# Kernel tuning notes

Hardware: AMD Instinct MI355X
Metric: run time of the kernel (lower is better)

## Reference

```python
import jax, jax.numpy as jnp
import numpy as np

N_NODES = 100000
N_EDGES = 1600000
INPUT_DIM, HIDDEN_DIM, OUTPUT_DIM = 128, 256, 2
BN_EPS = 1e-5


def setup_inputs() -> dict:
    key = jax.random.key(0)
    ks = jax.random.split(key, 8)
    x = jax.random.normal(ks[0], (N_NODES, INPUT_DIM), jnp.float32)
    edge_index = jax.random.randint(ks[1], (2, N_EDGES), 0, N_NODES, dtype=jnp.int32).astype(jnp.int64)
    # Glorot-ish init for GCNConv weights; PyG GCNConv has bias by default.
    def glorot(k, fan_in, fan_out):
        s = jnp.sqrt(6.0 / (fan_in + fan_out))
        return jax.random.uniform(k, (fan_in, fan_out), jnp.float32, -s, s)
    return {
        "x": x,
        "edge_index": edge_index,
        "W0": glorot(ks[2], INPUT_DIM, HIDDEN_DIM),
        "b0": jnp.zeros((HIDDEN_DIM,), jnp.float32),
        "W1": glorot(ks[3], HIDDEN_DIM, HIDDEN_DIM),
        "b1": jnp.zeros((HIDDEN_DIM,), jnp.float32),
        "W2": glorot(ks[4], HIDDEN_DIM, OUTPUT_DIM),
        "b2": jnp.zeros((OUTPUT_DIM,), jnp.float32),
        "gamma0": jnp.ones((HIDDEN_DIM,), jnp.float32),
        "beta0": jnp.zeros((HIDDEN_DIM,), jnp.float32),
        "gamma1": jnp.ones((HIDDEN_DIM,), jnp.float32),
        "beta1": jnp.zeros((HIDDEN_DIM,), jnp.float32),
    }


def _gcn_norm(edge_index, num_nodes):
    # PyG gcn_norm: add self-loops, deg over destination, D^-1/2 A_hat D^-1/2
    loop = jnp.arange(num_nodes, dtype=edge_index.dtype)
    src = jnp.concatenate([edge_index[0], loop])
    dst = jnp.concatenate([edge_index[1], loop])
    deg = jax.ops.segment_sum(jnp.ones_like(dst, jnp.float32), dst, num_segments=num_nodes)
    dinv = jax.lax.rsqrt(jnp.maximum(deg, 1.0))  # deg >= 1 due to self-loops
    norm = dinv[src] * dinv[dst]  # [E + N]
    return src, dst, norm


def _gcn_conv(x, W, b, src, dst, norm, num_nodes):
    h = x @ W                          # [N, out] dense GEMM first (PyG order)
    msg = h[src] * norm[:, None]       # gather + edge scale
    out = jax.ops.segment_sum(msg, dst, num_segments=num_nodes)  # scatter-add
    return out + b


def _batchnorm(x, gamma, beta):
    # training-mode BatchNorm1d over nodes (biased variance, as torch uses for normalization)
    mean = jnp.mean(x, axis=0)
    var = jnp.mean(jnp.square(x - mean), axis=0)
    return (x - mean) * jax.lax.rsqrt(var + BN_EPS) * gamma + beta


def reference(x, edge_index, W0, b0, W1, b1, W2, b2, gamma0, beta0, gamma1, beta1):
    n = x.shape[0]
    src, dst, norm = _gcn_norm(edge_index, n)
    h = _gcn_conv(x, W0, b0, src, dst, norm, n)
    h = jax.nn.relu(_batchnorm(h, gamma0, beta0))  # dropout is identity (eval / deterministic)
    h = _gcn_conv(h, W1, b1, src, dst, norm, n)
    h = jax.nn.relu(_batchnorm(h, gamma1, beta1))
    out = _gcn_conv(h, W2, b2, src, dst, norm, n)
    return out
```

## Files before the change

### kernel.cpp

```cpp
#include <hip/hip_runtime.h>
#include <hip/hip_fp16.h>


#define BN_EPS 1e-5f

union HF4 { float4 f; __half2 h[4]; };

typedef __attribute__((ext_vector_type(8))) _Float16 f16x8;
typedef __attribute__((ext_vector_type(4))) float f32x4;

__global__ void detect_i64(const unsigned int* __restrict__ w, int* flag) {
  __shared__ unsigned int red[256];
  unsigned int v = 0;
  int t = threadIdx.x;
  for (int i = t; i < 1024; i += 256) v |= w[2 * i + 1];
  red[t] = v;
  __syncthreads();
  for (int s = 128; s > 0; s >>= 1) {
    if (t < s) red[t] |= red[t + s];
    __syncthreads();
  }
  if (t == 0) *flag = (red[0] == 0u) ? 1 : 0;
}

__global__ void convert_deg(const unsigned int* __restrict__ w, const int* __restrict__ flag,
                            int* __restrict__ srcI, int* __restrict__ dstI,
                            int* __restrict__ deg, int E) {
  int i = blockIdx.x * blockDim.x + threadIdx.x;
  if (i >= E) return;
  int f = *flag;
  int s = (int)(f ? w[2 * (size_t)i] : w[i]);
  int d = (int)(f ? w[2 * ((size_t)E + i)] : w[(size_t)E + i]);
  srcI[i] = s;
  dstI[i] = d;
  atomicAdd(&deg[d], 1);
}

__global__ void make_dinv(const int* __restrict__ deg, float* __restrict__ dinv, int N) {
  int i = blockIdx.x * blockDim.x + threadIdx.x;
  if (i < N) dinv[i] = rsqrtf((float)deg[i] + 1.0f);
}

__global__ void scan_partial(const int* __restrict__ deg, int* __restrict__ blksum, int N) {
  __shared__ int s[256];
  int b = blockIdx.x, t = threadIdx.x;
  int base = b * 1024 + t * 4;
  int v = 0;
#pragma unroll
  for (int k = 0; k < 4; ++k) {
    int i = base + k;
    if (i < N) v += deg[i];
  }
  s[t] = v;
  __syncthreads();
  for (int st = 128; st > 0; st >>= 1) {
    if (t < st) s[t] += s[t + st];
    __syncthreads();
  }
  if (t == 0) blksum[b] = s[0];
}

__global__ void scan_blk(int* __restrict__ blksum, int B) {
  __shared__ int s[256];
  int t = threadIdx.x;
  int v = (t < B) ? blksum[t] : 0;
  s[t] = v;
  __syncthreads();
  for (int off = 1; off < 256; off <<= 1) {
    int u = (t >= off) ? s[t - off] : 0;
    __syncthreads();
    s[t] += u;
    __syncthreads();
  }
  if (t < B) blksum[t] = s[t] - v;
}

__global__ void scan_final(const int* __restrict__ deg, const int* __restrict__ blkoff,
                           int* __restrict__ rowptr, int N, int E) {
  __shared__ int s[256];
  int b = blockIdx.x, t = threadIdx.x;
  int base = b * 1024 + t * 4;
  int v[4];
  int sum = 0;
#pragma unroll
  for (int k = 0; k < 4; ++k) {
    int i = base + k;
    v[k] = (i < N) ? deg[i] : 0;
    sum += v[k];
  }
  s[t] = sum;
  __syncthreads();
  for (int off = 1; off < 256; off <<= 1) {
    int u = (t >= off) ? s[t - off] : 0;
    __syncthreads();
    s[t] += u;
    __syncthreads();
  }
  int ex = s[t] - sum + blkoff[b];
#pragma unroll
  for (int k = 0; k < 4; ++k) {
    int i = base + k;
    if (i < N) {
      rowptr[i] = ex;
      ex += v[k];
    }
  }
  if (b == 0 && t == 0) rowptr[N] = E;
}

__global__ void csr_scatter(const int* __restrict__ src, const int* __restrict__ dst,
                            const float* __restrict__ dinv, const int* __restrict__ rowptr,
                            int* __restrict__ fill, int* __restrict__ col,
                            float* __restrict__ wgt, int E) {
  int e = blockIdx.x * blockDim.x + threadIdx.x;
  if (e >= E) return;
  int s = src[e], d = dst[e];
  int pos = atomicAdd(&fill[d], 1);
  int slot = rowptr[d] + pos;
  col[slot] = s;
  wgt[slot] = dinv[s] * dinv[d];
}

__global__ void f32_to_f16(const float4* __restrict__ in, float4* __restrict__ outh, long n8) {
  long t = (long)blockIdx.x * blockDim.x + threadIdx.x;
  if (t >= n8) return;
  float4 a = in[2 * t], b = in[2 * t + 1];
  HF4 o;
  o.h[0] = __floats2half2_rn(a.x, a.y);
  o.h[1] = __floats2half2_rn(a.z, a.w);
  o.h[2] = __floats2half2_rn(b.x, b.y);
  o.h[3] = __floats2half2_rn(b.z, b.w);
  outh[t] = o.f;
}

__global__ void pack_w(const float* __restrict__ W, _Float16* __restrict__ Wp, int K, int NC) {
  int idx = blockIdx.x * blockDim.x + threadIdx.x;
  if (idx >= K * NC) return;
  int k = idx / NC, n = idx - k * NC;
  int kb = k >> 5, kk = k & 31, seg = kk >> 3, j = kk & 7;
  Wp[(((kb * 4 + seg) * NC) + n) * 8 + j] = (_Float16)W[idx];
}

template <int LPN>
__global__ void agg_gather_h(const float4* __restrict__ inh, float4* __restrict__ outh,
                             const int* __restrict__ rowptr, const int* __restrict__ col,
                             const float* __restrict__ wgt, const float* __restrict__ dinv,
                             int N) {
  long g = (long)blockIdx.x * blockDim.x + threadIdx.x;
  int n = (int)(g / LPN);
  int lane = (int)(g & (LPN - 1));
  if (n >= N) return;
  float ws = dinv[n];
  ws *= ws;
  float acc[8];
  {
    HF4 u;
    u.f = inh[(long)n * LPN + lane];
#pragma unroll
    for (int i = 0; i < 4; ++i) {
      float2 f = __half22float2(u.h[i]);
      acc[2 * i] = ws * f.x;
      acc[2 * i + 1] = ws * f.y;
    }
  }
  int beg = rowptr[n], end = rowptr[n + 1];
  int j = beg;
  for (; j + 3 < end; j += 4) {
    int s0 = col[j], s1 = col[j + 1], s2 = col[j + 2], s3 = col[j + 3];
    float w0 = wgt[j], w1 = wgt[j + 1], w2 = wgt[j + 2], w3 = wgt[j + 3];
    HF4 a, b, c, d;
    a.f = inh[(long)s0 * LPN + lane];
    b.f = inh[(long)s1 * LPN + lane];
    c.f = inh[(long)s2 * LPN + lane];
    d.f = inh[(long)s3 * LPN + lane];
#pragma unroll
    for (int i = 0; i < 4; ++i) {
      float2 fa = __half22float2(a.h[i]);
      float2 fb = __half22float2(b.h[i]);
      float2 fc = __half22float2(c.h[i]);
      float2 fd = __half22float2(d.h[i]);
      acc[2 * i] += w0 * fa.x + w1 * fb.x + w2 * fc.x + w3 * fd.x;
      acc[2 * i + 1] += w0 * fa.y + w1 * fb.y + w2 * fc.y + w3 * fd.y;
    }
  }
  for (; j < end; ++j) {
    int s0 = col[j];
    float w0 = wgt[j];
    HF4 a;
    a.f = inh[(long)s0 * LPN + lane];
#pragma unroll
    for (int i = 0; i < 4; ++i) {
      float2 fa = __half22float2(a.h[i]);
      acc[2 * i] += w0 * fa.x;
      acc[2 * i + 1] += w0 * fa.y;
    }
  }
  HF4 o;
  o.h[0] = __floats2half2_rn(acc[0], acc[1]);
  o.h[1] = __floats2half2_rn(acc[2], acc[3]);
  o.h[2] = __floats2half2_rn(acc[4], acc[5]);
  o.h[3] = __floats2half2_rn(acc[6], acc[7]);
  outh[(long)n * LPN + lane] = o.f;
}

template <int K, int NC>
__global__ __launch_bounds__(256) void gemm_mfma(const _Float16* __restrict__ A,
                                                 const float4* __restrict__ Wpack,
                                                 _Float16* __restrict__ H,
                                                 float* __restrict__ gsum,
                                                 float* __restrict__ gsq, int M) {
  __shared__ float red0[NC];
  __shared__ float red1[NC];
  int tid = threadIdx.x;
  if (tid < NC) {
    red0[tid] = 0.f;
    red1[tid] = 0.f;
  }
  __syncthreads();
  int wave = tid >> 6;
  int lane = tid & 63;
  int row0 = (blockIdx.x * 4 + wave) * 32;
  bool active = row0 < M;
  int arow0 = active ? row0 : 0;
  int r = lane & 15;
  int seg = lane >> 4;
  f32x4 acc0[NC / 16], acc1[NC / 16];
#pragma unroll
  for (int t = 0; t < NC / 16; ++t) {
    acc0[t] = (f32x4){0.f, 0.f, 0.f, 0.f};
    acc1[t] = (f32x4){0.f, 0.f, 0.f, 0.f};
  }
  const _Float16* arowA = A + (long)(arow0 + r) * K;
  const _Float16* arowB = A + (long)(arow0 + 16 + r) * K;
#pragma unroll
  for (int k0 = 0; k0 < K; k0 += 32) {
    f16x8 af0 = *(const f16x8*)(arowA + k0 + seg * 8);
    f16x8 af1 = *(const f16x8*)(arowB + k0 + seg * 8);
    const float4* wp = Wpack + ((k0 >> 5) * 4 + seg) * NC;
#pragma unroll
    for (int t = 0; t < NC / 16; ++t) {
      f16x8 bf = *(const f16x8*)(wp + t * 16 + r);
      acc0[t] = __builtin_amdgcn_mfma_f32_16x16x32_f16(af0, bf, acc0[t], 0, 0, 0);
      acc1[t] = __builtin_amdgcn_mfma_f32_16x16x32_f16(af1, bf, acc1[t], 0, 0, 0);
    }
  }
#pragma unroll
  for (int t = 0; t < NC / 16; ++t) {
    int c = t * 16 + r;
    float s = 0.f, q = 0.f;
#pragma unroll
    for (int qq = 0; qq < 4; ++qq) {
      float v0 = acc0[t][qq], v1 = acc1[t][qq];
      s += v0 + v1;
      q += v0 * v0 + v1 * v1;
    }
    s += __shfl_xor(s, 16, 64);
    s += __shfl_xor(s, 32, 64);
    q += __shfl_xor(q, 16, 64);
    q += __shfl_xor(q, 32, 64);
    if (active) {
      if (seg == 0) {
        atomicAdd(&red0[c], s);
        atomicAdd(&red1[c], q);
      }
#pragma unroll
      for (int qq = 0; qq < 4; ++qq) {
        H[(long)(row0 + seg * 4 + qq) * NC + c] = (_Float16)acc0[t][qq];
        H[(long)(row0 + 16 + seg * 4 + qq) * NC + c] = (_Float16)acc1[t][qq];
      }
    }
  }
  __syncthreads();
  if (tid < NC) {
    atomicAdd(&gsum[tid], red0[tid]);
    atomicAdd(&gsq[tid], red1[tid]);
  }
}

__global__ void bn_finalize(const float* __restrict__ gsum, const float* __restrict__ gsq,
                            const float* __restrict__ gamma, const float* __restrict__ beta,
                            float* __restrict__ scale, float* __restrict__ shift, float invN) {
  int c = threadIdx.x;
  float mean = gsum[c] * invN;
  float var = fmaxf(gsq[c] * invN - mean * mean, 0.f);
  float sc = rsqrtf(var + BN_EPS) * gamma[c];
  scale[c] = sc;
  shift[c] = beta[c] - mean * sc;
}

__global__ void bn_apply_h(const float4* __restrict__ h_in, float4* __restrict__ h_out,
                           const float4* __restrict__ scale4, const float4* __restrict__ shift4,
                           long total8) {
  long t = (long)blockIdx.x * blockDim.x + threadIdx.x;
  if (t >= total8) return;
  HF4 u;
  u.f = h_in[t];
  int c8 = (int)(t & 31);
  float4 sc0 = scale4[2 * c8], sh0 = shift4[2 * c8];
  float4 sc1 = scale4[2 * c8 + 1], sh1 = shift4[2 * c8 + 1];
  float2 f0 = __half22float2(u.h[0]);
  float2 f1 = __half22float2(u.h[1]);
  float2 f2 = __half22float2(u.h[2]);
  float2 f3 = __half22float2(u.h[3]);
  HF4 o;
  o.h[0] = __floats2half2_rn(fmaxf(f0.x * sc0.x + sh0.x, 0.f), fmaxf(f0.y * sc0.y + sh0.y, 0.f));
  o.h[1] = __floats2half2_rn(fmaxf(f1.x * sc0.z + sh0.z, 0.f), fmaxf(f1.y * sc0.w + sh0.w, 0.f));
  o.h[2] = __floats2half2_rn(fmaxf(f2.x * sc1.x + sh1.x, 0.f), fmaxf(f2.y * sc1.y + sh1.y, 0.f));
  o.h[3] = __floats2half2_rn(fmaxf(f3.x * sc1.z + sh1.z, 0.f), fmaxf(f3.y * sc1.w + sh1.w, 0.f));
  h_out[t] = o.f;
}

__global__ void bn_apply_proj(const float4* __restrict__ h_in, const float* __restrict__ scale,
                              const float* __restrict__ shift, const float* __restrict__ W2,
                              float* __restrict__ P, int N) {
  int tid = threadIdx.x;
  int row = blockIdx.x * 8 + (tid >> 5);
  int lr = tid & 31;
  if (row >= N) return;
  HF4 u;
  u.f = h_in[(long)row * 32 + lr];
  int c0 = lr * 8;
  float s0 = 0.f, s1 = 0.f;
#pragma unroll
  for (int i = 0; i < 4; ++i) {
    float2 f = __half22float2(u.h[i]);
    int ca = c0 + 2 * i, cb = c0 + 2 * i + 1;
    float va = fmaxf(f.x * scale[ca] + shift[ca], 0.f);
    float vb = fmaxf(f.y * scale[cb] + shift[cb], 0.f);
    s0 += va * W2[2 * ca] + vb * W2[2 * cb];
    s1 += va * W2[2 * ca + 1] + vb * W2[2 * cb + 1];
  }
#pragma unroll
  for (int off = 16; off > 0; off >>= 1) {
    s0 += __shfl_down(s0, off, 32);
    s1 += __shfl_down(s1, off, 32);
  }
  if (lr == 0) {
    P[2 * row] = s0;
    P[2 * row + 1] = s1;
  }
}

__global__ void final_gather(const float* __restrict__ P, float* __restrict__ out,
                             const int* __restrict__ rowptr, const int* __restrict__ col,
                             const float* __restrict__ wgt, const float* __restrict__ dinv,
                             const float* __restrict__ b2, int N) {
  int n = blockIdx.x * blockDim.x + threadIdx.x;
  if (n >= N) return;
  float w = dinv[n] * dinv[n];
  float a0 = w * P[2 * n + 0];
  float a1 = w * P[2 * n + 1];
  int end = rowptr[n + 1];
  for (int j = rowptr[n]; j < end; ++j) {
    int s = col[j];
    float ww = wgt[j];
    a0 += ww * P[2 * s + 0];
    a1 += ww * P[2 * s + 1];
  }
  out[2 * n + 0] = a0 + b2[0];
  out[2 * n + 1] = a1 + b2[1];
}

extern "C" void kernel_launch(void* const* d_in, const int* in_sizes, int n_in,
                              void* d_out, int out_size, void* d_ws, size_t ws_size,
                              hipStream_t stream) {
  const float* x = (const float*)d_in[0];
  const void* eidx = d_in[1];
  const float* W0 = (const float*)d_in[2];
  const float* W1 = (const float*)d_in[4];
  const float* W2 = (const float*)d_in[6];
  const float* b2 = (const float*)d_in[7];
  const float* gamma0 = (const float*)d_in[8];
  const float* beta0 = (const float*)d_in[9];
  const float* gamma1 = (const float*)d_in[10];
  const float* beta1 = (const float*)d_in[11];

  const int N = in_sizes[0] / 128;
  const int E = in_sizes[1] / 2;
  float* out = (float*)d_out;

  char* base = (char*)d_ws;
  size_t off = 0;
  auto alloc = [&](size_t bytes) {
    size_t o = off;
    off = (off + bytes + 255) & ~(size_t)255;
    return o;
  };
  const size_t o_col = alloc((size_t)E * 4);
  const size_t o_wgt = alloc((size_t)E * 4);
  const size_t o_rowptr = alloc((size_t)(N + 1) * 4);
  const size_t o_deg = alloc((size_t)N * 4);
  const size_t o_fill = alloc((size_t)N * 4);
  const size_t o_dinv = alloc((size_t)N * 4);
  const size_t o_blk = alloc(1024 * 4);
  const size_t o_flag = alloc(256);
  const size_t o_stats = alloc(4096);
  const size_t o_P = alloc((size_t)N * 2 * 4);
  const size_t o_W0p = alloc(128 * 256 * 2);
  const size_t o_W1p = alloc(256 * 256 * 2);
  const size_t o_H1 = alloc((size_t)N * 256 * 2);
  const size_t o_H2 = alloc((size_t)N * 256 * 2);

  int* col = (int*)(base + o_col);
  float* wgt = (float*)(base + o_wgt);
  int* rowptr = (int*)(base + o_rowptr);
  int* deg = (int*)(base + o_deg);
  int* fill = (int*)(base + o_fill);
  float* dinv = (float*)(base + o_dinv);
  int* blk = (int*)(base + o_blk);
  int* flag = (int*)(base + o_flag);
  float* gsum = (float*)(base + o_stats);
  float* gsq = gsum + 256;
  float* scale = gsum + 512;
  float* shift = gsum + 768;
  float* P = (float*)(base + o_P);
  _Float16* W0p = (_Float16*)(base + o_W0p);
  _Float16* W1p = (_Float16*)(base + o_W1p);
  float4* H1 = (float4*)(base + o_H1);
  float4* H2 = (float4*)(base + o_H2);
  int* idx32 = (int*)(base + o_H2);
  int* srcI = idx32;
  int* dstI = idx32 + E;

  auto cdiv = [](long a, long b) { return (int)((a + b - 1) / b); };
  const float invN = 1.0f / (float)N;
  const int B1 = cdiv(N, 1024);

  hipLaunchKernelGGL(detect_i64, dim3(1), dim3(256), 0, stream, (const unsigned int*)eidx, flag);
  hipMemsetAsync(deg, 0, (size_t)N * 4, stream);
  hipMemsetAsync(fill, 0, (size_t)N * 4, stream);
  hipLaunchKernelGGL(convert_deg, dim3(cdiv(E, 256)), dim3(256), 0, stream,
                     (const unsigned int*)eidx, flag, srcI, dstI, deg, E);

  hipLaunchKernelGGL(make_dinv, dim3(cdiv(N, 256)), dim3(256), 0, stream, deg, dinv, N);
  hipLaunchKernelGGL(scan_partial, dim3(B1), dim3(256), 0, stream, deg, blk, N);
  hipLaunchKernelGGL(scan_blk, dim3(1), dim3(256), 0, stream, blk, B1);
  hipLaunchKernelGGL(scan_final, dim3(B1), dim3(256), 0, stream, deg, blk, rowptr, N, E);
  hipLaunchKernelGGL(csr_scatter, dim3(cdiv(E, 256)), dim3(256), 0, stream, srcI, dstI, dinv,
                     rowptr, fill, col, wgt, E);
  hipLaunchKernelGGL(pack_w, dim3(cdiv(128 * 256, 256)), dim3(256), 0, stream, W0, W0p, 128, 256);
  hipLaunchKernelGGL(pack_w, dim3(cdiv(256 * 256, 256)), dim3(256), 0, stream, W1, W1p, 256, 256);
  hipLaunchKernelGGL(f32_to_f16, dim3(cdiv((long)N * 16, 256)), dim3(256), 0, stream,
                     (const float4*)x, H1, (long)N * 16);

  hipLaunchKernelGGL((agg_gather_h<16>), dim3(cdiv((long)N * 16, 256)), dim3(256), 0, stream,
                     H1, H2, rowptr, col, wgt, dinv, N);
  hipMemsetAsync(gsum, 0, 2048, stream);
  hipLaunchKernelGGL((gemm_mfma<128, 256>), dim3(cdiv(N, 128)), dim3(256), 0, stream,
                     (const _Float16*)H2, (const float4*)W0p, (_Float16*)H1, gsum, gsq, N);

  hipLaunchKernelGGL(bn_finalize, dim3(1), dim3(256), 0, stream, gsum, gsq, gamma0, beta0, scale,
                     shift, invN);
  hipLaunchKernelGGL(bn_apply_h, dim3(cdiv((long)N * 32, 256)), dim3(256), 0, stream,
                     (const float4*)H1, H2, (const float4*)scale, (const float4*)shift,
                     (long)N * 32);

  hipLaunchKernelGGL((agg_gather_h<32>), dim3(cdiv((long)N * 32, 256)), dim3(256), 0, stream,
                     H2, H1, rowptr, col, wgt, dinv, N);
  hipMemsetAsync(gsum, 0, 2048, stream);
  hipLaunchKernelGGL((gemm_mfma<256, 256>), dim3(cdiv(N, 128)), dim3(256), 0, stream,
                     (const _Float16*)H1, (const float4*)W1p, (_Float16*)H2, gsum, gsq, N);

  hipLaunchKernelGGL(bn_finalize, dim3(1), dim3(256), 0, stream, gsum, gsq, gamma1, beta1, scale,
                     shift, invN);
  hipLaunchKernelGGL(bn_apply_proj, dim3(cdiv(N, 8)), dim3(256), 0, stream, (const float4*)H2,
                     scale, shift, W2, P, N);

  hipLaunchKernelGGL(final_gather, dim3(cdiv(N, 256)), dim3(256), 0, stream, P, out, rowptr, col,
                     wgt, dinv, b2, N);
}
```

Baseline: 597.5 us.

## Fuse BN-apply into gather, split BN stats from GEMM, drop index conversion

Several changes land together. The int32 src/dst conversion pass is removed, so the degree count and CSR scatter read the raw edge index directly. The BN statistics reduction moves out of the MFMA GEMM epilogue into a separate bn_stats kernel. The GEMM operands are swapped so each lane writes four contiguous fp16 values instead of scalar strided stores. The layer-0 BN+ReLU apply is folded into the second aggregation's loads, removing a full read/write pass of the hidden activations. The cost is one extra read of the GEMM output for stats, and the BN transform is now recomputed once per edge gather instead of once per node.

After: 664.0 us. 1.11x slower.

```diff
diff --git a/kernel.cpp b/kernel.cpp
--- a/kernel.cpp
+++ b/kernel.cpp
@@ -5,6 +5,7 @@
 #define BN_EPS 1e-5f
 
 union HF4 { float4 f; __half2 h[4]; };
+union HF2 { float2 f; __half2 h[2]; };
 
 typedef __attribute__((ext_vector_type(8))) _Float16 f16x8;
 typedef __attribute__((ext_vector_type(4))) float f32x4;
@@ -23,21 +24,19 @@
   if (t == 0) *flag = (red[0] == 0u) ? 1 : 0;
 }
 
-__global__ void convert_deg(const unsigned int* __restrict__ w, const int* __restrict__ flag,
-                            int* __restrict__ srcI, int* __restrict__ dstI,
-                            int* __restrict__ deg, int E) {
+__global__ void deg_count(const unsigned int* __restrict__ w, const int* __restrict__ flag,
+                          int* __restrict__ deg, int E) {
   int i = blockIdx.x * blockDim.x + threadIdx.x;
   if (i >= E) return;
   int f = *flag;
-  int s = (int)(f ? w[2 * (size_t)i] : w[i]);
   int d = (int)(f ? w[2 * ((size_t)E + i)] : w[(size_t)E + i]);
-  srcI[i] = s;
-  dstI[i] = d;
   atomicAdd(&deg[d], 1);
 }
 
-__global__ void make_dinv(const int* __restrict__ deg, float* __restrict__ dinv, int N) {
+__global__ void make_dinv(const int* __restrict__ deg, float* __restrict__ dinv,
+                          float* __restrict__ stats, int N) {
   int i = blockIdx.x * blockDim.x + threadIdx.x;
+  if (i < 512) stats[i] = 0.f;
   if (i < N) dinv[i] = rsqrtf((float)deg[i] + 1.0f);
 }
 
@@ -108,13 +107,15 @@
   if (b == 0 && t == 0) rowptr[N] = E;
 }
 
-__global__ void csr_scatter(const int* __restrict__ src, const int* __restrict__ dst,
+__global__ void csr_scatter(const unsigned int* __restrict__ w, const int* __restrict__ flag,
                             const float* __restrict__ dinv, const int* __restrict__ rowptr,
                             int* __restrict__ fill, int* __restrict__ col,
                             float* __restrict__ wgt, int E) {
   int e = blockIdx.x * blockDim.x + threadIdx.x;
   if (e >= E) return;
-  int s = src[e], d = dst[e];
+  int f = *flag;
+  int s = (int)(f ? w[2 * (size_t)e] : w[e]);
+  int d = (int)(f ? w[2 * ((size_t)E + e)] : w[(size_t)E + e]);
   int pos = atomicAdd(&fill[d], 1);
   int slot = rowptr[d] + pos;
   col[slot] = s;
@@ -141,27 +142,46 @@
   Wp[(((kb * 4 + seg) * NC) + n) * 8 + j] = (_Float16)W[idx];
 }
 
-template <int LPN>
+template <int LPN, bool BN>
 __global__ void agg_gather_h(const float4* __restrict__ inh, float4* __restrict__ outh,
                              const int* __restrict__ rowptr, const int* __restrict__ col,
                              const float* __restrict__ wgt, const float* __restrict__ dinv,
+                             const float* __restrict__ scale, const float* __restrict__ shift,
                              int N) {
   long g = (long)blockIdx.x * blockDim.x + threadIdx.x;
   int n = (int)(g / LPN);
   int lane = (int)(g & (LPN - 1));
   if (n >= N) return;
+  float sc[8], sh[8];
+  if (BN) {
+    int c0 = lane * 8;
+#pragma unroll
+    for (int i = 0; i < 8; ++i) {
+      sc[i] = scale[c0 + i];
+      sh[i] = shift[c0 + i];
+    }
+  }
+  auto xf = [&](const HF4& u, float* o) {
+#pragma unroll
+    for (int i = 0; i < 4; ++i) {
+      float2 f = __half22float2(u.h[i]);
+      o[2 * i] = f.x;
+      o[2 * i + 1] = f.y;
+    }
+    if (BN) {
+#pragma unroll
+      for (int i = 0; i < 8; ++i) o[i] = fmaxf(o[i] * sc[i] + sh[i], 0.f);
+    }
+  };
   float ws = dinv[n];
   ws *= ws;
-  float acc[8];
+  float acc[8], v[8];
   {
     HF4 u;
     u.f = inh[(long)n * LPN + lane];
-#pragma unroll
-    for (int i = 0; i < 4; ++i) {
-      float2 f = __half22float2(u.h[i]);
-      acc[2 * i] = ws * f.x;
-      acc[2 * i + 1] = ws * f.y;
-    }
+    xf(u, v);
+#pragma unroll
+    for (int i = 0; i < 8; ++i) acc[i] = ws * v[i];
   }
   int beg = rowptr[n], end = rowptr[n + 1];
   int j = beg;
@@ -173,27 +193,21 @@
     b.f = inh[(long)s1 * LPN + lane];
     c.f = inh[(long)s2 * LPN + lane];
     d.f = inh[(long)s3 * LPN + lane];
-#pragma unroll
-    for (int i = 0; i < 4; ++i) {
-      float2 fa = __half22float2(a.h[i]);
-      float2 fb = __half22float2(b.h[i]);
-      float2 fc = __half22float2(c.h[i]);
-      float2 fd = __half22float2(d.h[i]);
-      acc[2 * i] += w0 * fa.x + w1 * fb.x + w2 * fc.x + w3 * fd.x;
-      acc[2 * i + 1] += w0 * fa.y + w1 * fb.y + w2 * fc.y + w3 * fd.y;
-    }
+    float va[8], vb[8], vc[8], vd[8];
+    xf(a, va); xf(b, vb); xf(c, vc); xf(d, vd);
+#pragma unroll
+    for (int i = 0; i < 8; ++i)
+      acc[i] += w0 * va[i] + w1 * vb[i] + w2 * vc[i] + w3 * vd[i];
   }
   for (; j < end; ++j) {
     int s0 = col[j];
     float w0 = wgt[j];
     HF4 a;
     a.f = inh[(long)s0 * LPN + lane];
-#pragma unroll
-    for (int i = 0; i < 4; ++i) {
-      float2 fa = __half22float2(a.h[i]);
-      acc[2 * i] += w0 * fa.x;
-      acc[2 * i + 1] += w0 * fa.y;
-    }
+    float va[8];
+    xf(a, va);
+#pragma unroll
+    for (int i = 0; i < 8; ++i) acc[i] += w0 * va[i];
   }
   HF4 o;
   o.h[0] = __floats2half2_rn(acc[0], acc[1]);
@@ -206,22 +220,12 @@
 template <int K, int NC>
 __global__ __launch_bounds__(256) void gemm_mfma(const _Float16* __restrict__ A,
                                                  const float4* __restrict__ Wpack,
-                                                 _Float16* __restrict__ H,
-                                                 float* __restrict__ gsum,
-                                                 float* __restrict__ gsq, int M) {
-  __shared__ float red0[NC];
-  __shared__ float red1[NC];
+                                                 _Float16* __restrict__ H, int M) {
   int tid = threadIdx.x;
-  if (tid < NC) {
-    red0[tid] = 0.f;
-    red1[tid] = 0.f;
-  }
-  __syncthreads();
   int wave = tid >> 6;
   int lane = tid & 63;
   int row0 = (blockIdx.x * 4 + wave) * 32;
-  bool active = row0 < M;
-  int arow0 = active ? row0 : 0;
+  if (row0 >= M) return;
   int r = lane & 15;
   int seg = lane >> 4;
   f32x4 acc0[NC / 16], acc1[NC / 16];
@@ -230,54 +234,66 @@
     acc0[t] = (f32x4){0.f, 0.f, 0.f, 0.f};
     acc1[t] = (f32x4){0.f, 0.f, 0.f, 0.f};
   }
-  const _Float16* arowA = A + (long)(arow0 + r) * K;
-  const _Float16* arowB = A + (long)(arow0 + 16 + r) * K;
+  int ra = min(row0 + r, M - 1);
+  int rb = min(row0 + 16 + r, M - 1);
+  const _Float16* arowA = A + (long)ra * K;
+  const _Float16* arowB = A + (long)rb * K;
 #pragma unroll
   for (int k0 = 0; k0 < K; k0 += 32) {
-    f16x8 af0 = *(const f16x8*)(arowA + k0 + seg * 8);
-    f16x8 af1 = *(const f16x8*)(arowB + k0 + seg * 8);
+    f16x8 hf0 = *(const f16x8*)(arowA + k0 + seg * 8);
+    f16x8 hf1 = *(const f16x8*)(arowB + k0 + seg * 8);
     const float4* wp = Wpack + ((k0 >> 5) * 4 + seg) * NC;
 #pragma unroll
     for (int t = 0; t < NC / 16; ++t) {
-      f16x8 bf = *(const f16x8*)(wp + t * 16 + r);
-      acc0[t] = __builtin_amdgcn_mfma_f32_16x16x32_f16(af0, bf, acc0[t], 0, 0, 0);
-      acc1[t] = __builtin_amdgcn_mfma_f32_16x16x32_f16(af1, bf, acc1[t], 0, 0, 0);
-    }
-  }
+      f16x8 wf = *(const f16x8*)(wp + t * 16 + r);
+      acc0[t] = __builtin_amdgcn_mfma_f32_16x16x32_f16(wf, hf0, acc0[t], 0, 0, 0);
+      acc1[t] = __builtin_amdgcn_mfma_f32_16x16x32_f16(wf, hf1, acc1[t], 0, 0, 0);
+    }
+  }
+  bool okA = row0 + r < M, okB = row0 + 16 + r < M;
+  _Float16* hA = H + (long)(row0 + r) * NC + seg * 4;
+  _Float16* hB = H + (long)(row0 + 16 + r) * NC + seg * 4;
 #pragma unroll
   for (int t = 0; t < NC / 16; ++t) {
-    int c = t * 16 + r;
-    float s = 0.f, q = 0.f;
-#pragma unroll
-    for (int qq = 0; qq < 4; ++qq) {
-      float v0 = acc0[t][qq], v1 = acc1[t][qq];
-      s += v0 + v1;
-      q += v0 * v0 + v1 * v1;
-    }
-    s += __shfl_xor(s, 16, 64);
-    s += __shfl_xor(s, 32, 64);
-    q += __shfl_xor(q, 16, 64);
-    q += __shfl_xor(q, 32, 64);
-    if (active) {
-      if (seg == 0) {
-        atomicAdd(&red0[c], s);
-        atomicAdd(&red1[c], q);
-      }
-#pragma unroll
-      for (int qq = 0; qq < 4; ++qq) {
-        H[(long)(row0 + seg * 4 + qq) * NC + c] = (_Float16)acc0[t][qq];
-        H[(long)(row0 + 16 + seg * 4 + qq) * NC + c] = (_Float16)acc1[t][qq];
-      }
-    }
-  }
+    if (okA) {
+      HF2 o;
+      o.h[0] = __floats2half2_rn(acc0[t][0], acc0[t][1]);
+      o.h[1] = __floats2half2_rn(acc0[t][2], acc0[t][3]);
+      *(float2*)(hA + t * 16) = o.f;
+    }
+    if (okB) {
+      HF2 o;
+      o.h[0] = __floats2half2_rn(acc1[t][0], acc1[t][1]);
+      o.h[1] = __floats2half2_rn(acc1[t][2], acc1[t][3]);
+      *(float2*)(hB + t * 16) = o.f;
+    }
+  }
+}
+
+__global__ void bn_stats_h(const __half2* __restrict__ x, float* __restrict__ gsum,
+                           float* __restrict__ gsq, int N) {
+  __shared__ float rs[2][256], rq[2][256];
+  int tid = threadIdx.x;
+  int c2 = tid & 127;
+  int rg = tid >> 7;
+  int r0 = blockIdx.x * 512 + rg;
+  int r1 = min(blockIdx.x * 512 + 512, N);
+  float s0 = 0.f, s1 = 0.f, q0 = 0.f, q1 = 0.f;
+  for (int r = r0; r < r1; r += 2) {
+    float2 f = __half22float2(x[(long)r * 128 + c2]);
+    s0 += f.x; s1 += f.y;
+    q0 += f.x * f.x; q1 += f.y * f.y;
+  }
+  rs[rg][2 * c2] = s0; rs[rg][2 * c2 + 1] = s1;
+  rq[rg][2 * c2] = q0; rq[rg][2 * c2 + 1] = q1;
   __syncthreads();
-  if (tid < NC) {
-    atomicAdd(&gsum[tid], red0[tid]);
-    atomicAdd(&gsq[tid], red1[tid]);
-  }
-}
-
-__global__ void bn_finalize(const float* __restrict__ gsum, const float* __restrict__ gsq,
+  if (tid < 256) {
+    atomicAdd(&gsum[tid], rs[0][tid] + rs[1][tid]);
+    atomicAdd(&gsq[tid], rq[0][tid] + rq[1][tid]);
+  }
+}
+
+__global__ void bn_finalize(float* __restrict__ gsum, float* __restrict__ gsq,
                             const float* __restrict__ gamma, const float* __restrict__ beta,
                             float* __restrict__ scale, float* __restrict__ shift, float invN) {
   int c = threadIdx.x;
@@ -286,28 +302,8 @@
   float sc = rsqrtf(var + BN_EPS) * gamma[c];
   scale[c] = sc;
   shift[c] = beta[c] - mean * sc;
-}
-
-__global__ void bn_apply_h(const float4* __restrict__ h_in, float4* __restrict__ h_out,
-                           const float4* __restrict__ scale4, const float4* __restrict__ shift4,
-                           long total8) {
-  long t = (long)blockIdx.x * blockDim.x + threadIdx.x;
-  if (t >= total8) return;
-  HF4 u;
-  u.f = h_in[t];
-  int c8 = (int)(t & 31);
-  float4 sc0 = scale4[2 * c8], sh0 = shift4[2 * c8];
-  float4 sc1 = scale4[2 * c8 + 1], sh1 = shift4[2 * c8 + 1];
-  float2 f0 = __half22float2(u.h[0]);
-  float2 f1 = __half22float2(u.h[1]);
-  float2 f2 = __half22float2(u.h[2]);
-  float2 f3 = __half22float2(u.h[3]);
-  HF4 o;
-  o.h[0] = __floats2half2_rn(fmaxf(f0.x * sc0.x + sh0.x, 0.f), fmaxf(f0.y * sc0.y + sh0.y, 0.f));
-  o.h[1] = __floats2half2_rn(fmaxf(f1.x * sc0.z + sh0.z, 0.f), fmaxf(f1.y * sc0.w + sh0.w, 0.f));
-  o.h[2] = __floats2half2_rn(fmaxf(f2.x * sc1.x + sh1.x, 0.f), fmaxf(f2.y * sc1.y + sh1.y, 0.f));
-  o.h[3] = __floats2half2_rn(fmaxf(f3.x * sc1.z + sh1.z, 0.f), fmaxf(f3.y * sc1.w + sh1.w, 0.f));
-  h_out[t] = o.f;
+  gsum[c] = 0.f;
+  gsq[c] = 0.f;
 }
 
 __global__ void bn_apply_proj(const float4* __restrict__ h_in, const float* __restrict__ scale,
@@ -365,7 +361,7 @@
                               void* d_out, int out_size, void* d_ws, size_t ws_size,
                               hipStream_t stream) {
   const float* x = (const float*)d_in[0];
-  const void* eidx = d_in[1];
+  const unsigned int* eidx = (const unsigned int*)d_in[1];
   const float* W0 = (const float*)d_in[2];
   const float* W1 = (const float*)d_in[4];
   const float* W2 = (const float*)d_in[6];
@@ -418,52 +414,47 @@
   _Float16* W1p = (_Float16*)(base + o_W1p);
   float4* H1 = (float4*)(base + o_H1);
   float4* H2 = (float4*)(base + o_H2);
-  int* idx32 = (int*)(base + o_H2);
-  int* srcI = idx32;
-  int* dstI = idx32 + E;
 
   auto cdiv = [](long a, long b) { return (int)((a + b - 1) / b); };
   const float invN = 1.0f / (float)N;
   const int B1 = cdiv(N, 1024);
 
-  hipLaunchKernelGGL(detect_i64, dim3(1), dim3(256), 0, stream, (const unsigned int*)eidx, flag);
+  hipLaunchKernelGGL(detect_i64, dim3(1), dim3(256), 0, stream, eidx, flag);
   hipMemsetAsync(deg, 0, (size_t)N * 4, stream);
   hipMemsetAsync(fill, 0, (size_t)N * 4, stream);
-  hipLaunchKernelGGL(convert_deg, dim3(cdiv(E, 256)), dim3(256), 0, stream,
-                     (const unsigned int*)eidx, flag, srcI, dstI, deg, E);
-
-  hipLaunchKernelGGL(make_dinv, dim3(cdiv(N, 256)), dim3(256), 0, stream, deg, dinv, N);
+  hipLaunchKernelGGL(deg_count, dim3(cdiv(E, 256)), dim3(256), 0, stream, eidx, flag, deg, E);
+
+  hipLaunchKernelGGL(make_dinv, dim3(cdiv(N, 256)), dim3(256), 0, stream, deg, dinv, gsum, N);
   hipLaunchKernelGGL(scan_partial, dim3(B1), dim3(256), 0, stream, deg, blk, N);
   hipLaunchKernelGGL(scan_blk, dim3(1), dim3(256), 0, stream, blk, B1);
   hipLaunchKernelGGL(scan_final, dim3(B1), dim3(256), 0, stream, deg, blk, rowptr, N, E);
-  hipLaunchKernelGGL(csr_scatter, dim3(cdiv(E, 256)), dim3(256), 0, stream, srcI, dstI, dinv,
+  hipLaunchKernelGGL(csr_scatter, dim3(cdiv(E, 256)), dim3(256), 0, stream, eidx, flag, dinv,
                      rowptr, fill, col, wgt, E);
   hipLaunchKernelGGL(pack_w, dim3(cdiv(128 * 256, 256)), dim3(256), 0, stream, W0, W0p, 128, 256);
   hipLaunchKernelGGL(pack_w, dim3(cdiv(256 * 256, 256)), dim3(256), 0, stream, W1, W1p, 256, 256);
   hipLaunchKernelGGL(f32_to_f16, dim3(cdiv((long)N * 16, 256)), dim3(256), 0, stream,
                      (const float4*)x, H1, (long)N * 16);
 
-  hipLaunchKernelGGL((agg_gather_h<16>), dim3(cdiv((long)N * 16, 256)), dim3(256), 0, stream,
-                     H1, H2, rowptr, col, wgt, dinv, N);
-  hipMemsetAsync(gsum, 0, 2048, stream);
+  hipLaunchKernelGGL((agg_gather_h<16, false>), dim3(cdiv((long)N * 16, 256)), dim3(256), 0,
+                     stream, H1, H2, rowptr, col, wgt, dinv, nullptr, nullptr, N);
   hipLaunchKernelGGL((gemm_mfma<128, 256>), dim3(cdiv(N, 128)), dim3(256), 0, stream,
-                     (const _Float16*)H2, (const float4*)W0p, (_Float16*)H1, gsum, gsq, N);
-
+                     (const _Float16*)H2, (const float4*)W0p, (_Float16*)H1, N);
+
+  hipLaunchKernelGGL(bn_stats_h, dim3(cdiv(N, 512)), dim3(256), 0, stream, (const __half2*)H1,
+                     gsum, gsq, N);
   hipLaunchKernelGGL(bn_finalize, dim3(1), dim3(256), 0, stream, gsum, gsq, gamma0, beta0, scale,
                      shift, invN);
-  hipLaunchKernelGGL(bn_apply_h, dim3(cdiv((long)N * 32, 256)), dim3(256), 0, stream,
-                     (const float4*)H1, H2, (const float4*)scale, (const float4*)shift,
-                     (long)N * 32);
-
-  hipLaunchKernelGGL((agg_gather_h<32>), dim3(cdiv((long)N * 32, 256)), dim3(256), 0, stream,
-                     H2, H1, rowptr, col, wgt, dinv, N);
-  hipMemsetAsync(gsum, 0, 2048, stream);
+
+  hipLaunchKernelGGL((agg_gather_h<32, true>), dim3(cdiv((long)N * 32, 256)), dim3(256), 0,
+                     stream, H1, H2, rowptr, col, wgt, dinv, scale, shift, N);
   hipLaunchKernelGGL((gemm_mfma<256, 256>), dim3(cdiv(N, 128)), dim3(256), 0, stream,
-                     (const _Float16*)H1, (const float4*)W1p, (_Float16*)H2, gsum, gsq, N);
-
+                     (const _Float16*)H2, (const float4*)W1p, (_Float16*)H1, N);
+
+  hipLaunchKernelGGL(bn_stats_h, dim3(cdiv(N, 512)), dim3(256), 0, stream, (const __half2*)H1,
+                     gsum, gsq, N);
   hipLaunchKernelGGL(bn_finalize, dim3(1), dim3(256), 0, stream, gsum, gsq, gamma1, beta1, scale,
                      shift, invN);
-  hipLaunchKernelGGL(bn_apply_proj, dim3(cdiv(N, 8)), dim3(256), 0, stream, (const float4*)H2,
+  hipLaunchKernelGGL(bn_apply_proj, dim3(cdiv(N, 8)), dim3(256), 0, stream, (const float4*)H1,
                      scale, shift, W2, P, N);
 
   hipLaunchKernelGGL(final_gather, dim3(cdiv(N, 256)), dim3(256), 0, stream, P, out, rowptr, col,
```
